# Performance work log

Measured on AMD Instinct MI355X. Metric: run time of the kernel, lower is better.

## Reference

```python
import jax, jax.numpy as jnp
import numpy as np

KERNEL_MUL = 10.0
KERNEL_NUM = 5


def _multi_kernel(dist, n_samples):
    # bandwidth estimated from detached distances (torch uses .data)
    bw = jax.lax.stop_gradient(jnp.sum(dist)) / (n_samples * n_samples - n_samples)
    bw = bw / (KERNEL_MUL ** (KERNEL_NUM // 2))
    k = jnp.zeros_like(dist)
    for i in range(KERNEL_NUM):
        k = k + jnp.exp(-dist / (bw * KERNEL_MUL ** i))
    return k


def setup_inputs() -> dict:
    key = jax.random.key(0)
    k1, k2 = jax.random.split(key)
    B, D = 256, 512
    source = jax.random.normal(k1, (B, D), dtype=jnp.float32)
    target = jax.random.normal(k2, (B, D), dtype=jnp.float32)
    return {"source": source, "target": target}


def reference(source, target):
    B = source.shape[0]
    src = source.reshape(B, -1)
    tgt = target.reshape(target.shape[0], -1)
    total = jnp.concatenate([src, tgt], axis=0)  # [N, D], N = 2B
    N = total.shape[0]

    # L2 pairwise distances via norm expansion (avoids [N,N,D] intermediate)
    sq = jnp.sum(total * total, axis=1)  # [N]
    L2 = jnp.maximum(sq[:, None] + sq[None, :] - 2.0 * (total @ total.T), 0.0)

    # L1 pairwise distances (structurally needs pairwise diffs)
    L1 = jnp.sum(jnp.abs(total[:, None, :] - total[None, :, :]), axis=-1)  # [N, N]

    kernels = _multi_kernel(L2, N) + _multi_kernel(L1, N)

    XX = kernels[:B, :B]
    YY = kernels[B:, B:]
    XY = kernels[:B, B:]
    YX = kernels[B:, :B]
    return jnp.mean(XX + YY - XY - YX)
```

## Files before the change

kernel.cpp:

```cpp
#include <hip/hip_runtime.h>

#define NROWS 512
#define BHALF 256
#define DIM   512
#define TILE  64
#define DCHUNK 64
#define NCHUNK 8
#define NN (NROWS * NROWS)
#define SOFF (16 * NN)


#define ACC(A, Bb, IV, JV)                                    \
    {                                                         \
        const float d_ = (IV) - (JV);                         \
        a2[A][Bb] = fmaf(d_, d_, a2[A][Bb]);                  \
        a1[A][Bb] += fabsf(d_);                               \
    }

#define STEP(DD)                                              \
    {                                                         \
        const float4 ivv = *(const float4*)&ai[DD][ty4];      \
        const float4 jvv = *(const float4*)&aj[DD][tx4];      \
        ACC(0, 0, ivv.x, jvv.x) ACC(0, 1, ivv.x, jvv.y)       \
        ACC(0, 2, ivv.x, jvv.z) ACC(0, 3, ivv.x, jvv.w)       \
        ACC(1, 0, ivv.y, jvv.x) ACC(1, 1, ivv.y, jvv.y)       \
        ACC(1, 2, ivv.y, jvv.z) ACC(1, 3, ivv.y, jvv.w)       \
        ACC(2, 0, ivv.z, jvv.x) ACC(2, 1, ivv.z, jvv.y)       \
        ACC(2, 2, ivv.z, jvv.z) ACC(2, 3, ivv.z, jvv.w)       \
        ACC(3, 0, ivv.w, jvv.x) ACC(3, 1, ivv.w, jvv.y)       \
        ACC(3, 2, ivv.w, jvv.z) ACC(3, 3, ivv.w, jvv.w)       \
    }

__global__ __launch_bounds__(256) void k_dist(const float* __restrict__ src,
                                              const float* __restrict__ tgt,
                                              float* __restrict__ ws)
{
    __shared__ float ai[DCHUNK][TILE];
    __shared__ float aj[DCHUNK][TILE];

    const int tj = blockIdx.x;
    const int ti = blockIdx.y;
    const int dc = blockIdx.z;
    const int t  = threadIdx.x;

    {
        const int r  = t & 63;
        const int dg = t >> 6;
        const int gi = ti * TILE + r;
        const int gj = tj * TILE + r;
        const float* prow_i = (gi < BHALF ? src + (size_t)gi * DIM
                                          : tgt + (size_t)(gi - BHALF) * DIM) + dc * DCHUNK;
        const float* prow_j = (gj < BHALF ? src + (size_t)gj * DIM
                                          : tgt + (size_t)(gj - BHALF) * DIM) + dc * DCHUNK;
#pragma unroll
        for (int k = 0; k < 4; ++k) {
            const int d4 = dg * 4 + k;
            const float4 vi = *(const float4*)(prow_i + d4 * 4);
            const float4 vj = *(const float4*)(prow_j + d4 * 4);
            ai[d4 * 4 + 0][r] = vi.x; ai[d4 * 4 + 1][r] = vi.y;
            ai[d4 * 4 + 2][r] = vi.z; ai[d4 * 4 + 3][r] = vi.w;
            aj[d4 * 4 + 0][r] = vj.x; aj[d4 * 4 + 1][r] = vj.y;
            aj[d4 * 4 + 2][r] = vj.z; aj[d4 * 4 + 3][r] = vj.w;
        }
    }
    __syncthreads();

    const int tx  = t & 15;
    const int ty  = t >> 4;
    const int tx4 = tx * 4;
    const int ty4 = ty * 4;

    float a2[4][4], a1[4][4];
#pragma unroll
    for (int a = 0; a < 4; ++a)
#pragma unroll
        for (int b = 0; b < 4; ++b) { a2[a][b] = 0.f; a1[a][b] = 0.f; }

#pragma unroll 4
    for (int d = 0; d < DCHUNK; d += 2) {
        STEP(d)
        STEP(d + 1)
    }

    float* part2 = ws + (size_t)dc * NN;
    float* part1 = ws + (size_t)(NCHUNK + dc) * NN;
    const int gj0 = tj * TILE + tx4;
#pragma unroll
    for (int a = 0; a < 4; ++a) {
        const int gi = ti * TILE + ty4 + a;
        const float4 s2 = make_float4(a2[a][0], a2[a][1], a2[a][2], a2[a][3]);
        const float4 s1 = make_float4(a1[a][0], a1[a][1], a1[a][2], a1[a][3]);
        *(float4*)&part2[(size_t)gi * NROWS + gj0] = s2;
        *(float4*)&part1[(size_t)gi * NROWS + gj0] = s1;
    }

    float s2 = 0.f, s1 = 0.f;
#pragma unroll
    for (int a = 0; a < 4; ++a)
#pragma unroll
        for (int b = 0; b < 4; ++b) { s2 += a2[a][b]; s1 += a1[a][b]; }
#pragma unroll
    for (int off = 32; off > 0; off >>= 1) {
        s2 += __shfl_down(s2, off);
        s1 += __shfl_down(s1, off);
    }
    __syncthreads();
    float* red = &ai[0][0];
    const int wave = t >> 6;
    if ((t & 63) == 0) { red[wave * 2] = s2; red[wave * 2 + 1] = s1; }
    __syncthreads();
    if (t == 0) {
        const int bid = (dc * 8 + ti) * 8 + tj;
        ws[SOFF + bid]       = red[0] + red[2] + red[4] + red[6];
        ws[SOFF + 512 + bid] = red[1] + red[3] + red[5] + red[7];
    }
}

__global__ __launch_bounds__(256) void k_mmd(const float* __restrict__ ws,
                                             float* __restrict__ out)
{
    const int t = threadIdx.x;
    __shared__ float sred[8];

    float sp2 = ws[SOFF + t] + ws[SOFF + 256 + t];
    float sp1 = ws[SOFF + 512 + t] + ws[SOFF + 768 + t];
#pragma unroll
    for (int off = 32; off > 0; off >>= 1) {
        sp2 += __shfl_down(sp2, off);
        sp1 += __shfl_down(sp1, off);
    }
    if ((t & 63) == 0) { sred[(t >> 6) * 2] = sp2; sred[(t >> 6) * 2 + 1] = sp1; }
    __syncthreads();
    const float S2 = sred[0] + sred[2] + sred[4] + sred[6];
    const float S1 = sred[1] + sred[3] + sred[5] + sred[7];
    const float r2 = 26163200.0f / S2;
    const float r1 = 26163200.0f / S1;

    float acc = 0.f;
    const int base = blockIdx.x * 1024 + t;
#pragma unroll
    for (int q = 0; q < 4; ++q) {
        const int idx = base + q * 256;
        float l2 = 0.f, l1 = 0.f;
#pragma unroll
        for (int c = 0; c < NCHUNK; ++c) {
            l2 += ws[(size_t)c * NN + idx];
            l1 += ws[(size_t)(NCHUNK + c) * NN + idx];
        }
        float kv = 0.f;
        float f2 = r2, f1 = r1;
#pragma unroll
        for (int tt = 0; tt < 5; ++tt) {
            kv += __expf(-l2 * f2) + __expf(-l1 * f1);
            f2 *= 0.1f;
            f1 *= 0.1f;
        }
        const int i = idx >> 9;
        const int j = idx & 511;
        const float sgn = (((i ^ j) & BHALF) == 0) ? 1.0f : -1.0f;
        acc += sgn * kv;
    }
#pragma unroll
    for (int off = 32; off > 0; off >>= 1) acc += __shfl_down(acc, off);

    __syncthreads();
    if ((t & 63) == 0) sred[t >> 6] = acc;
    __syncthreads();
    if (t == 0) {
        const float s = sred[0] + sred[1] + sred[2] + sred[3];
        atomicAdd(out, s * (1.0f / 65536.0f));
    }
}

extern "C" void kernel_launch(void* const* d_in, const int* in_sizes, int n_in,
                              void* d_out, int out_size, void* d_ws, size_t ws_size,
                              hipStream_t stream)
{
    const float* src = (const float*)d_in[0];
    const float* tgt = (const float*)d_in[1];
    float* ws  = (float*)d_ws;
    float* out = (float*)d_out;

    hipMemsetAsync(out, 0, sizeof(float), stream);

    dim3 g1(8, 8, 8);
    k_dist<<<g1, 256, 0, stream>>>(src, tgt, ws);
    k_mmd<<<256, 256, 0, stream>>>(ws, out);
}
```

Before: 83.23 us.

## Store per-chunk partial distances as packed fp16 and fold output zeroing into kernel

Partial L2 and L1 distance sums for each D-chunk are now written as a packed half2 per element instead of two fp32 arrays, halving the workspace write and read traffic between the two kernels. The output memset is replaced by a store from one thread of the first kernel, removing a separate launch. The cost is precision: partial sums are rounded to fp16 before being accumulated and fed into the exponentials. Values near 128 for L2 partials are representable, but the rounding error can shift the final MMD value.

```diff
diff --git a/kernel.cpp b/kernel.cpp
--- a/kernel.cpp
+++ b/kernel.cpp
@@ -1,4 +1,5 @@
 #include <hip/hip_runtime.h>
+#include <hip/hip_fp16.h>
 
 #define NROWS 512
 #define BHALF 256
@@ -7,8 +8,7 @@
 #define DCHUNK 64
 #define NCHUNK 8
 #define NN (NROWS * NROWS)
-#define SOFF (16 * NN)
-
+#define SOFF (8 * NN)
 
 #define ACC(A, Bb, IV, JV)                                    \
     {                                                         \
@@ -31,9 +31,16 @@
         ACC(3, 2, ivv.w, jvv.z) ACC(3, 3, ivv.w, jvv.w)       \
     }
 
+__device__ __forceinline__ unsigned int pack_h2(float l2v, float l1v) {
+    const __half2 h = __halves2half2(__float2half_rn(l2v), __float2half_rn(l1v));
+    union { __half2 h; unsigned int u; } c; c.h = h;
+    return c.u;
+}
+
 __global__ __launch_bounds__(256) void k_dist(const float* __restrict__ src,
                                               const float* __restrict__ tgt,
-                                              float* __restrict__ ws)
+                                              float* __restrict__ ws,
+                                              float* __restrict__ out)
 {
     __shared__ float ai[DCHUNK][TILE];
     __shared__ float aj[DCHUNK][TILE];
@@ -42,6 +49,8 @@
     const int ti = blockIdx.y;
     const int dc = blockIdx.z;
     const int t  = threadIdx.x;
+
+    if (t == 0 && tj == 0 && ti == 0 && dc == 0) out[0] = 0.0f;
 
     {
         const int r  = t & 63;
@@ -82,16 +91,16 @@
         STEP(d + 1)
     }
 
-    float* part2 = ws + (size_t)dc * NN;
-    float* part1 = ws + (size_t)(NCHUNK + dc) * NN;
+    unsigned int* part = (unsigned int*)ws + (size_t)dc * NN;
     const int gj0 = tj * TILE + tx4;
 #pragma unroll
     for (int a = 0; a < 4; ++a) {
         const int gi = ti * TILE + ty4 + a;
-        const float4 s2 = make_float4(a2[a][0], a2[a][1], a2[a][2], a2[a][3]);
-        const float4 s1 = make_float4(a1[a][0], a1[a][1], a1[a][2], a1[a][3]);
-        *(float4*)&part2[(size_t)gi * NROWS + gj0] = s2;
-        *(float4*)&part1[(size_t)gi * NROWS + gj0] = s1;
+        const uint4 pk = make_uint4(pack_h2(a2[a][0], a1[a][0]),
+                                    pack_h2(a2[a][1], a1[a][1]),
+                                    pack_h2(a2[a][2], a1[a][2]),
+                                    pack_h2(a2[a][3], a1[a][3]));
+        *(uint4*)&part[(size_t)gi * NROWS + gj0] = pk;
     }
 
     float s2 = 0.f, s1 = 0.f;
@@ -136,6 +145,8 @@
     const float r2 = 26163200.0f / S2;
     const float r1 = 26163200.0f / S1;
 
+    const __half2* part = (const __half2*)ws;
+
     float acc = 0.f;
     const int base = blockIdx.x * 1024 + t;
 #pragma unroll
@@ -144,8 +155,9 @@
         float l2 = 0.f, l1 = 0.f;
 #pragma unroll
         for (int c = 0; c < NCHUNK; ++c) {
-            l2 += ws[(size_t)c * NN + idx];
-            l1 += ws[(size_t)(NCHUNK + c) * NN + idx];
+            const float2 f = __half22float2(part[(size_t)c * NN + idx]);
+            l2 += f.x;
+            l1 += f.y;
         }
         float kv = 0.f;
         float f2 = r2, f1 = r1;
@@ -181,9 +193,7 @@
     float* ws  = (float*)d_ws;
     float* out = (float*)d_out;
 
-    hipMemsetAsync(out, 0, sizeof(float), stream);
-
     dim3 g1(8, 8, 8);
-    k_dist<<<g1, 256, 0, stream>>>(src, tgt, ws);
+    k_dist<<<g1, 256, 0, stream>>>(src, tgt, ws, out);
     k_mmd<<<256, 256, 0, stream>>>(ws, out);
 }
```

New measurement: 78.82 us. 5.3% less time.
